# Performance work log

Hardware: AMD Instinct MI355X
Metric: run time of the kernel (lower is better)

## Reference

```python
import jax, jax.numpy as jnp
import numpy as np

# ---- static config (from MACEConfig / MACELayerConfig) ----
N_NODES = 128
F_S = 128          # n_invariant_feat_hidden (0e channels)
F_V = 64           # n_vectors_hidden (1e channels)
N_BESSEL = 8       # bessel_number
R_MAX = 5.0        # r_max
N_LAYERS = 2       # n_interactions
HID_RAD = 64       # radial MLP hidden width
F_S_OUT = 128      # n_invariant_feat_readout
F_V_OUT = 64       # n_vectors_readout
AVG_NEIGH = float(N_NODES)  # avg_num_neighbors default = n_nodes
RAD_OUT = F_S + 3 * F_V     # per-edge radial channel weights for the 4 TP paths


def _senders_receivers(n):
    # fully connected graph, matching get_senders_and_receivers
    s = np.repeat(np.arange(n), n - 1)
    j = np.tile(np.arange(1, n), n)
    r = (s + j) % n
    return jnp.asarray(s, dtype=jnp.int32), jnp.asarray(r, dtype=jnp.int32)


def _bessel(r):
    # e3nn bessel basis: sqrt(2/c) sin(n pi r / c) / r, n = 1..N_BESSEL
    n = jnp.arange(1, N_BESSEL + 1, dtype=r.dtype)
    return jnp.sqrt(2.0 / R_MAX) * jnp.sin(n * jnp.pi * r[:, None] / R_MAX) / r[:, None]


def _envelope(r):
    # smooth radial cutoff (polynomial p=6), stand-in for e3nn soft_envelope
    u = r / R_MAX
    p = 6.0
    env = 1.0 - (p + 1) * (p + 2) / 2 * u ** p + p * (p + 2) * u ** (p + 1) - p * (p + 1) / 2 * u ** (p + 2)
    return jnp.where(u < 1.0, env, 0.0)


def _forward(x, species_embed, Wr1, Wr2, W_sv, W_mix_s, W_mix_v, W_out_s, W_out_v):
    senders, receivers = _senders_receivers(N_NODES)

    def single(pos):  # pos: (N, 3)
        com = pos.mean(axis=0)                       # centre of mass (3,)
        v = pos[receivers] - pos[senders]            # edge relative vectors (E, 3)
        r = jnp.linalg.norm(v, axis=-1) + 1e-8       # (E,)
        vhat = v / r[:, None]
        rb = _bessel(r) * _envelope(r)[:, None]      # (E, N_BESSEL)

        s = jnp.broadcast_to(species_embed[0], (N_NODES, F_S))       # 0e node feats
        V = jnp.zeros((N_NODES, F_V, 3), dtype=pos.dtype)            # 1e node feats

        for l in range(N_LAYERS):
            # learned per-edge radial weights for each tensor-product path
            h = jax.nn.silu(rb @ Wr1[l]) @ Wr2[l]    # (E, RAD_OUT)
            R0 = h[:, :F_S]
            R1 = h[:, F_S:F_S + F_V]
            R2 = h[:, F_S + F_V:F_S + 2 * F_V]
            R3 = h[:, F_S + 2 * F_V:]

            s_src = s[senders]                       # gather (E, F_S)
            V_src = V[senders]                       # gather (E, F_V, 3)

            # CG tensor-product paths (only 0e and 1e irreps present):
            m0a = R0 * s_src                                         # 0e x 0e -> 0e
            m0b = R1 * jnp.einsum('efk,ek->ef', V_src, vhat)         # 1e x 1e -> 0e
            m1a = (R2 * (s_src @ W_sv[l]))[..., None] * vhat[:, None, :]  # 0e x 1e -> 1e
            m1b = R3[..., None] * V_src                              # 1e x 0e -> 1e

            # scatter-sum message passing over receivers
            agg0 = jax.ops.segment_sum(jnp.concatenate([m0a, m0b], -1), receivers,
                                       num_segments=N_NODES) / AVG_NEIGH   # (N, F_S+F_V)
            agg1 = jax.ops.segment_sum(jnp.concatenate([m1a, m1b], 1), receivers,
                                       num_segments=N_NODES) / AVG_NEIGH   # (N, 2F_V, 3)

            s = s + jax.nn.silu(agg0 @ W_mix_s[l])
            V = V + jnp.einsum('nfk,fg->ngk', agg1, W_mix_v[l])

        out_s = s @ W_out_s                                          # (N, F_S_OUT)
        out_v = jnp.einsum('nfk,fg->ngk', V, W_out_v) + com          # (N, F_V_OUT, 3) + CoM
        return out_v, out_s

    return jax.vmap(single)(x)


def setup_inputs() -> dict:
    key = jax.random.key(0)
    ks = jax.random.split(key, 10)
    sc = lambda fan: 1.0 / np.sqrt(fan)
    inp = {
        'x': jax.random.normal(ks[0], (8, N_NODES, 3), dtype=jnp.float32),
        'species_embed': jax.random.normal(ks[1], (1, F_S), dtype=jnp.float32),
        'Wr1': jax.random.normal(ks[2], (N_LAYERS, N_BESSEL, HID_RAD), dtype=jnp.float32) * sc(N_BESSEL),
        'Wr2': jax.random.normal(ks[3], (N_LAYERS, HID_RAD, RAD_OUT), dtype=jnp.float32) * sc(HID_RAD),
        'W_sv': jax.random.normal(ks[4], (N_LAYERS, F_S, F_V), dtype=jnp.float32) * sc(F_S),
        'W_mix_s': jax.random.normal(ks[5], (N_LAYERS, F_S + F_V, F_S), dtype=jnp.float32) * sc(F_S + F_V),
        'W_mix_v': jax.random.normal(ks[6], (N_LAYERS, 2 * F_V, F_V), dtype=jnp.float32) * sc(2 * F_V),
        'W_out_s': jax.random.normal(ks[7], (F_S, F_S_OUT), dtype=jnp.float32) * sc(F_S),
        'W_out_v': jax.random.normal(ks[8], (F_V, F_V_OUT), dtype=jnp.float32) * sc(F_V),
    }
    return inp


def reference(x, species_embed, Wr1, Wr2, W_sv, W_mix_s, W_mix_v, W_out_s, W_out_v):
    return _forward(x, species_embed, Wr1, Wr2, W_sv, W_mix_s, W_mix_v, W_out_s, W_out_v)
```

## Files before the change

kernel.cpp:

```cpp
#include <hip/hip_runtime.h>
#include <math.h>

typedef unsigned short u16;
typedef __attribute__((ext_vector_type(8))) short frag_ab;
typedef __attribute__((ext_vector_type(4))) float frag_cd;

#define BATCH 8
#define NN 128
#define FS 128
#define FV 64
#define NB 8
#define HID 64
#define ROUT 320
#define HSTRB 72

#define SZ_S (BATCH*FS*NN)
#define SZ_V (BATCH*FV*3*NN)
#define SZ_T (BATCH*FV*NN)
#define N_W2B (ROUT*HID)
#define OFF_SB 0
#define OFF_VB (OFF_SB+SZ_S)
#define OFF_T1 (OFF_VB+SZ_V)
#define OFF_W2B (OFF_T1+SZ_T)

// ... 154 lines not shown
    const int g = tid - 320;
    float a0=0.f, a1=0.f;
    #pragma unroll 8
    for (int c=0; c<FS; c+=2){
      a0 = fmaf(species[c],   Wsv[c*FV+g],     a0);
      a1 = fmaf(species[c+1], Wsv[(c+1)*FV+g], a1);
    }
    t0L[g] = a0+a1;
  } else if (tid < 424){
    const int t = blockIdx.x*40 + (tid-384);
    const int j = t & 63, c = t >> 6;
    w2b[t] = f2bf(Wr2[HID*ROUT + j*ROUT + c]);
  }
  __syncthreads();

  if (tid < FS){
    float a0=0.f, a1=0.f;
    #pragma unroll 2
    for (int c0=0; c0<128; c0+=4){
      float4 g0 = *(const float4*)&aggS[0][c0];
      float4 g1 = *(const float4*)&aggS[1][c0];
      float w0 = WmixSl[c0*FS+tid];
      float w1 = WmixSl[(c0+1)*FS+tid];
      float w2 = WmixSl[(c0+2)*FS+tid];
      float w3 = WmixSl[(c0+3)*FS+tid];
      a0 = fmaf(g0.x,w0,a0); a0 = fmaf(g0.y,w1,a0); a0 = fmaf(g0.z,w2,a0); a0 = fmaf(g0.w,w3,a0);
      a1 = fmaf(g1.x,w0,a1); a1 = fmaf(g1.y,w1,a1); a1 = fmaf(g1.z,w2,a1); a1 = fmaf(g1.w,w3,a1);
    }
    float sn0 = species[tid] + silu_f(a0);
    float sn1 = species[tid] + silu_f(a1);
    sNew[0][tid] = sn0;
    sNew[1][tid] = sn1;
    sOut[(b*FS+tid)*NN + k0]     = sn0;
    sOut[(b*FS+tid)*NN + k0 + 1] = sn1;
  } else if (tid < 320){
    const int o = tid - 128;
    const int g = o/3, c3 = o - g*3;
    float a0=0.f, a1=0.f;
    #pragma unroll 2
    for (int f0=0; f0<FV; f0+=4){
      float4 dv0 = *(const float4*)&dV[0][c3*68+f0];
      float4 dv1 = *(const float4*)&dV[1][c3*68+f0];
      float4 t4  = *(const float4*)&t0L[f0];
      float w0 = WmixVl[f0*FV+g];
      float w1 = WmixVl[(f0+1)*FV+g];
      float w2 = WmixVl[(f0+2)*FV+g];
      float w3 = WmixVl[(f0+3)*FV+g];
      a0 = fmaf(t4.x*dv0.x, w0, a0); a0 = fmaf(t4.y*dv0.y, w1, a0);
      a0 = fmaf(t4.z*dv0.z, w2, a0); a0 = fmaf(t4.w*dv0.w, w3, a0);
      a1 = fmaf(t4.x*dv1.x, w0, a1); a1 = fmaf(t4.y*dv1.y, w1, a1);
      a1 = fmaf(t4.z*dv1.z, w2, a1); a1 = fmaf(t4.w*dv1.w, w3, a1);
    }
    vOut[(b*FV*3 + o)*NN + k0]     = a0;
    vOut[(b*FV*3 + o)*NN + k0 + 1] = a1;
  }
  __syncthreads();

  if (tid < 256){
    const int g = tid & 63, p = tid >> 6;
    const float* Wsv1 = Wsv + FS*FV;
    const int f0 = p*32;
    float a0=0.f, a1=0.f;
    #pragma unroll 2
    for (int f=f0; f<f0+32; f+=4){
      float4 s0 = *(const float4*)&sNew[0][f];
      float4 s1 = *(const float4*)&sNew[1][f];
      float w0 = Wsv1[f*FV+g];
      float w1 = Wsv1[(f+1)*FV+g];
      float w2 = Wsv1[(f+2)*FV+g];
      float w3 = Wsv1[(f+3)*FV+g];
      a0 = fmaf(s0.x,w0,a0); a0 = fmaf(s0.y,w1,a0); a0 = fmaf(s0.z,w2,a0); a0 = fmaf(s0.w,w3,a0);
      a1 = fmaf(s1.x,w0,a1); a1 = fmaf(s1.y,w1,a1); a1 = fmaf(s1.z,w2,a1); a1 = fmaf(s1.w,w3,a1);
    }
    tPart[p][0][g] = a0; tPart[p][1][g] = a1;
  }
  __syncthreads();
  if (tid < 128){
    const int g = tid & 63, kk = tid >> 6;
    tOut[(b*FV+g)*NN + k0 + kk] =
        tPart[0][kk][g] + tPart[1][kk][g] + tPart[2][kk][g] + tPart[3][kk][g];
  }
}

__global__ __launch_bounds__(1024, 4) void layer_kernel(
    const float* __restrict__ pos,
    const float* __restrict__ sIn,
    const float* __restrict__ vIn,
    const float* __restrict__ tIn,
    const float* __restrict__ Wr1l,
    const u16*   __restrict__ w2bl,
    const float* __restrict__ WmixSl,
    const float* __restrict__ WmixVl,
    const float* __restrict__ WoutS,
    const float* __restrict__ WoutV,
    float* __restrict__ outp)
{
  const int tid  = threadIdx.x;
  const int b    = blockIdx.x >> 5;
  const int k0   = (blockIdx.x & 31) * 4;
  const int w    = tid >> 6;
  const int lane = tid & 63;
  const int col  = lane & 15;
  const int quad = lane >> 4;
  const int gh   = w & 1;
  const int wq   = (w >> 1) & 3;
  const int sh   = w >> 3;

  __shared__ u16   hidB[4][128*HSTRB];
  __shared__ float vhx[4][128], vhy[4][128], vhz[4][128];
  __shared__ float aggP[4][2][600];
  __shared__ float sPart[4][4][FS];
  __shared__ float sNew[4][FS];
  __shared__ float vNewL[4][204];
  __shared__ float comL[3];

  const float* pb = pos + b*NN*3;

  {
    const int jh = tid >> 9;
    const int kk = (tid >> 7) & 3;
    const int i  = tid & 127;
    const int k  = k0 + kk;
    float vx = pb[k*3+0]-pb[i*3+0];
    float vy = pb[k*3+1]-pb[i*3+1];
    float vz = pb[k*3+2]-pb[i*3+2];
    float r = sqrtf(vx*vx+vy*vy+vz*vz) + 1e-8f;
    float inv = 1.0f/r;
    if (jh == 0){ vhx[kk][i]=vx*inv; vhy[kk][i]=vy*inv; vhz[kk][i]=vz*inv; }
    float u = r*0.2f;
    float env = 0.0f;
    if (u < 1.0f && i != k){
      float u2=u*u, u6=u2*u2*u2;
      env = 1.0f - 28.0f*u6 + 48.0f*u6*u - 21.0f*u6*u2;
    }
    float coef = 0.6324555320336759f * inv * env;
    float th   = r * 0.6283185307179586f;
    float s1 = __sinf(th), c1 = __cosf(th);
    float rb[NB];
    rb[0] = coef*s1;
    float twoc = 2.f*c1, sp = s1, spp = 0.f;
    #pragma unroll
    for(int n=1;n<NB;n++){ float s = twoc*sp - spp; spp = sp; sp = s; rb[n] = coef*s; }
    u16* hrow = hidB[kk] + i*HSTRB;
    #pragma unroll
    for(int jg0=0;jg0<8;jg0++){
      const int jg = jh*8 + jg0;
      float h0=0.f,h1=0.f,h2=0.f,h3=0.f;
      #pragma unroll
      for(int n=0;n<NB;n++){
        const float* wr = Wr1l + n*HID + jg*4;
        float rn = rb[n];
        h0 = fmaf(rn, wr[0], h0);
        h1 = fmaf(rn, wr[1], h1);
        h2 = fmaf(rn, wr[2], h2);
        h3 = fmaf(rn, wr[3], h3);
      }
      ushort4 uu = make_ushort4(f2bf(silu_f(h0)), f2bf(silu_f(h1)),
                                f2bf(silu_f(h2)), f2bf(silu_f(h3)));
      *(ushort4*)(hrow + jg*4) = uu;
    }
    if (tid < 3){
      float a0=0.f, a1=0.f;
      for (int n=0;n<NN;n+=2){ a0 += pb[n*3+tid]; a1 += pb[(n+1)*3+tid]; }
      comL[tid] = (a0+a1) * (1.0f/128.0f);
    }
  }
  __syncthreads();

  const float* sIb = sIn + b*FS*NN;
  const float* vIb = vIn + b*FV*3*NN;
  const float* tIb = tIn + b*FV*NN;
  const int i00 = sh*64 + quad*4;

  if (gh == 0){
    const int c_s0 = wq*16 + col;
    const int c_s1 = 64 + c_s0;

    const u16* wp0 = w2bl + c_s0*HID + quad*8;
    const u16* wp1 = w2bl + c_s1*HID + quad*8;
    const u16* wp2 = w2bl + (128 + c_s0)*HID + quad*8;
    const frag_ab b00 = *(const frag_ab*)(wp0), b01 = *(const frag_ab*)(wp0+32);
    const frag_ab b10 = *(const frag_ab*)(wp1), b11 = *(const frag_ab*)(wp1+32);
    const frag_ab b20 = *(const frag_ab*)(wp2), b21 = *(const frag_ab*)(wp2+32);

    const float* fs0 = sIb + c_s0*NN + i00;
    const float* fs1 = sIb + c_s1*NN + i00;
    const float* fv  = vIb + c_s0*3*NN + i00;

    float sA0[4]={0.f,0.f,0.f,0.f}, sA1[4]={0.f,0.f,0.f,0.f}, sA2[4]={0.f,0.f,0.f,0.f};

    #pragma unroll 1
    for (int mt=0; mt<4; mt++){
      float4 s4a = *(const float4*)&fs0[mt*16];
      float4 s4b = *(const float4*)&fs1[mt*16];
      float4 vx4 = *(const float4*)&fv[mt*16];
      float4 vy4 = *(const float4*)&fv[NN + mt*16];
      float4 vz4 = *(const float4*)&fv[2*NN + mt*16];
      const int hbase = (sh*64 + mt*16 + col)*HSTRB + quad*8;
      const int vbase = i00 + mt*16;
      #pragma unroll
      for (int kk=0; kk<4; kk++){
        frag_ab a0 = *(const frag_ab*)&hidB[kk][hbase];
        frag_ab a1 = *(const frag_ab*)&hidB[kk][hbase + 32];
        float4 hx4 = *(const float4*)&vhx[kk][vbase];
        float4 hy4 = *(const float4*)&vhy[kk][vbase];
        float4 hz4 = *(const float4*)&vhz[kk][vbase];
        frag_cd ac0 = {0.f,0.f,0.f,0.f};
        frag_cd ac1 = {0.f,0.f,0.f,0.f};
        frag_cd ac2 = {0.f,0.f,0.f,0.f};
        ac0 = __builtin_amdgcn_mfma_f32_16x16x32_bf16(a0, b00, ac0, 0,0,0);
        ac1 = __builtin_amdgcn_mfma_f32_16x16x32_bf16(a0, b10, ac1, 0,0,0);
        ac2 = __builtin_amdgcn_mfma_f32_16x16x32_bf16(a0, b20, ac2, 0,0,0);
        ac0 = __builtin_amdgcn_mfma_f32_16x16x32_bf16(a1, b01, ac0, 0,0,0);
        ac1 = __builtin_amdgcn_mfma_f32_16x16x32_bf16(a1, b11, ac1, 0,0,0);
        ac2 = __builtin_amdgcn_mfma_f32_16x16x32_bf16(a1, b21, ac2, 0,0,0);

        sA0[kk] += ac0[0]*s4a.x + ac0[1]*s4a.y + ac0[2]*s4a.z + ac0[3]*s4a.w;
        sA1[kk] += ac1[0]*s4b.x + ac1[1]*s4b.y + ac1[2]*s4b.z + ac1[3]*s4b.w;
        sA2[kk] += ac2[0]*(vx4.x*hx4.x + vy4.x*hy4.x + vz4.x*hz4.x)
                 + ac2[1]*(vx4.y*hx4.y + vy4.y*hy4.y + vz4.y*hz4.y)
                 + ac2[2]*(vx4.z*hx4.z + vy4.z*hy4.z + vz4.z*hz4.z)
                 + ac2[3]*(vx4.w*hx4.w + vy4.w*hy4.w + vz4.w*hz4.w);
      }
    }
    #pragma unroll
    for (int kk=0; kk<4; kk++){
      float v0 = sA0[kk]; v0 += __shfl_xor(v0,16,64); v0 += __shfl_xor(v0,32,64);
      float v1 = sA1[kk]; v1 += __shfl_xor(v1,16,64); v1 += __shfl_xor(v1,32,64);
      float v2 = sA2[kk]; v2 += __shfl_xor(v2,16,64); v2 += __shfl_xor(v2,32,64);
      if (lane < 16){
        aggP[kk][sh][wq*16 + lane]       = v0;
        aggP[kk][sh][64 + wq*16 + lane]  = v1;
        aggP[kk][sh][128 + wq*16 + lane] = v2;
      }
    }
  } else {
    const int f_vc = wq*16 + col;

    const u16* wp3 = w2bl + (192 + f_vc)*HID + quad*8;
    const u16* wp4 = w2bl + (256 + f_vc)*HID + quad*8;
    const frag_ab b30 = *(const frag_ab*)(wp3), b31 = *(const frag_ab*)(wp3+32);
    const frag_ab b40 = *(const frag_ab*)(wp4), b41 = *(const frag_ab*)(wp4+32);

    const float* fv = vIb + f_vc*3*NN + i00;
    const float* ft = tIb + f_vc*NN + i00;

    float sX3[4]={0.f,0.f,0.f,0.f}, sY3[4]={0.f,0.f,0.f,0.f}, sZ3[4]={0.f,0.f,0.f,0.f};
    float sX4[4]={0.f,0.f,0.f,0.f}, sY4[4]={0.f,0.f,0.f,0.f}, sZ4[4]={0.f,0.f,0.f,0.f};

    #pragma unroll 1
    for (int mt=0; mt<4; mt++){
      float4 vx4 = *(const float4*)&fv[mt*16];
      float4 vy4 = *(const float4*)&fv[NN + mt*16];
      float4 vz4 = *(const float4*)&fv[2*NN + mt*16];
      float4 t4  = *(const float4*)&ft[mt*16];
      const int hbase = (sh*64 + mt*16 + col)*HSTRB + quad*8;
      const int vbase = i00 + mt*16;
      #pragma unroll
      for (int kk=0; kk<4; kk++){
        frag_ab a0 = *(const frag_ab*)&hidB[kk][hbase];
        frag_ab a1 = *(const frag_ab*)&hidB[kk][hbase + 32];
        float4 hx4 = *(const float4*)&vhx[kk][vbase];
        float4 hy4 = *(const float4*)&vhy[kk][vbase];
        float4 hz4 = *(const float4*)&vhz[kk][vbase];
        frag_cd ac3 = {0.f,0.f,0.f,0.f};
        frag_cd ac4 = {0.f,0.f,0.f,0.f};
        ac3 = __builtin_amdgcn_mfma_f32_16x16x32_bf16(a0, b30, ac3, 0,0,0);
        ac4 = __builtin_amdgcn_mfma_f32_16x16x32_bf16(a0, b40, ac4, 0,0,0);
        ac3 = __builtin_amdgcn_mfma_f32_16x16x32_bf16(a1, b31, ac3, 0,0,0);
        ac4 = __builtin_amdgcn_mfma_f32_16x16x32_bf16(a1, b41, ac4, 0,0,0);

        float t0_ = ac3[0]*t4.x, t1_ = ac3[1]*t4.y, t2_ = ac3[2]*t4.z, t3_ = ac3[3]*t4.w;
        sX3[kk] += t0_*hx4.x + t1_*hx4.y + t2_*hx4.z + t3_*hx4.w;
        sY3[kk] += t0_*hy4.x + t1_*hy4.y + t2_*hy4.z + t3_*hy4.w;
        sZ3[kk] += t0_*hz4.x + t1_*hz4.y + t2_*hz4.z + t3_*hz4.w;
        sX4[kk] += ac4[0]*vx4.x + ac4[1]*vx4.y + ac4[2]*vx4.z + ac4[3]*vx4.w;
        sY4[kk] += ac4[0]*vy4.x + ac4[1]*vy4.y + ac4[2]*vy4.z + ac4[3]*vy4.w;
        sZ4[kk] += ac4[0]*vz4.x + ac4[1]*vz4.y + ac4[2]*vz4.z + ac4[3]*vz4.w;
      }
    }
    #pragma unroll
    for (int kk=0; kk<4; kk++){
      float x3 = sX3[kk]; x3 += __shfl_xor(x3,16,64); x3 += __shfl_xor(x3,32,64);
      float y3 = sY3[kk]; y3 += __shfl_xor(y3,16,64); y3 += __shfl_xor(y3,32,64);
      float z3 = sZ3[kk]; z3 += __shfl_xor(z3,16,64); z3 += __shfl_xor(z3,32,64);
      float x4 = sX4[kk]; x4 += __shfl_xor(x4,16,64); x4 += __shfl_xor(x4,32,64);
      float y4 = sY4[kk]; y4 += __shfl_xor(y4,16,64); y4 += __shfl_xor(y4,32,64);
      float z4 = sZ4[kk]; z4 += __shfl_xor(z4,16,64); z4 += __shfl_xor(z4,32,64);
      if (lane < 16){
        const int f2 = wq*16 + lane;
        aggP[kk][sh][192       + f2] = x3;
        aggP[kk][sh][192 +  68 + f2] = y3;
        aggP[kk][sh][192 + 136 + f2] = z3;
        aggP[kk][sh][396       + f2] = x4;
        aggP[kk][sh][396 +  68 + f2] = y4;
        aggP[kk][sh][396 + 136 + f2] = z4;
      }
    }
  }

  __syncthreads();
  for (int t2=tid; t2<2400; t2+=1024){
    const int kk = t2 / 600;
    const int t  = t2 - kk*600;
    aggP[kk][0][t] = (aggP[kk][0][t] + aggP[kk][1][t]) * (1.0f/128.0f);
  }
  __syncthreads();

  if (tid < 512){
    const int o = tid & 127, p = tid >> 7;
    const int c0 = p*48;
    float a0=0.f,a1=0.f,a2=0.f,a3=0.f;
    #pragma unroll 2
    for (int cc=c0; cc<c0+48; cc+=4){
      float4 g0 = *(const float4*)&aggP[0][0][cc];
      float4 g1 = *(const float4*)&aggP[1][0][cc];
      float4 g2 = *(const float4*)&aggP[2][0][cc];
      float4 g3 = *(const float4*)&aggP[3][0][cc];
      float w0 = WmixSl[cc*FS+o];
      float w1 = WmixSl[(cc+1)*FS+o];
      float w2 = WmixSl[(cc+2)*FS+o];
      float w3 = WmixSl[(cc+3)*FS+o];
      a0 = fmaf(g0.x,w0,a0); a0 = fmaf(g0.y,w1,a0); a0 = fmaf(g0.z,w2,a0); a0 = fmaf(g0.w,w3,a0);
      a1 = fmaf(g1.x,w0,a1); a1 = fmaf(g1.y,w1,a1); a1 = fmaf(g1.z,w2,a1); a1 = fmaf(g1.w,w3,a1);
      a2 = fmaf(g2.x,w0,a2); a2 = fmaf(g2.y,w1,a2); a2 = fmaf(g2.z,w2,a2); a2 = fmaf(g2.w,w3,a2);
      a3 = fmaf(g3.x,w0,a3); a3 = fmaf(g3.y,w1,a3); a3 = fmaf(g3.z,w2,a3); a3 = fmaf(g3.w,w3,a3);
    }
    sPart[0][p][o] = a0; sPart[1][p][o] = a1;
    sPart[2][p][o] = a2; sPart[3][p][o] = a3;
  } else if (tid < 704){
    const int o = tid - 512;
    const int c3 = o >> 6, g = o & 63;
    float a0=0.f,a1=0.f,a2=0.f,a3=0.f;
    #pragma unroll 1
    for (int f0=0; f0<FV; f0+=4){
      float4 p0 = *(const float4*)&aggP[0][0][192+c3*68+f0];
      float4 q0 = *(const float4*)&aggP[0][0][396+c3*68+f0];
      float4 p1 = *(const float4*)&aggP[1][0][192+c3*68+f0];
      float4 q1 = *(const float4*)&aggP[1][0][396+c3*68+f0];
      float4 p2 = *(const float4*)&aggP[2][0][192+c3*68+f0];
      float4 q2 = *(const float4*)&aggP[2][0][396+c3*68+f0];
      float4 p3 = *(const float4*)&aggP[3][0][192+c3*68+f0];
      float4 q3 = *(const float4*)&aggP[3][0][396+c3*68+f0];
      float w00 = WmixVl[f0*FV+g];
      float w01 = WmixVl[(f0+1)*FV+g];
      float w02 = WmixVl[(f0+2)*FV+g];
      float w03 = WmixVl[(f0+3)*FV+g];
      float w10 = WmixVl[(f0+FV)*FV+g];
      float w11 = WmixVl[(f0+FV+1)*FV+g];
      float w12 = WmixVl[(f0+FV+2)*FV+g];
      float w13 = WmixVl[(f0+FV+3)*FV+g];
      a0 = fmaf(p0.x,w00,a0); a0 = fmaf(p0.y,w01,a0); a0 = fmaf(p0.z,w02,a0); a0 = fmaf(p0.w,w03,a0);
      a0 = fmaf(q0.x,w10,a0); a0 = fmaf(q0.y,w11,a0); a0 = fmaf(q0.z,w12,a0); a0 = fmaf(q0.w,w13,a0);
      a1 = fmaf(p1.x,w00,a1); a1 = fmaf(p1.y,w01,a1); a1 = fmaf(p1.z,w02,a1); a1 = fmaf(p1.w,w03,a1);
      a1 = fmaf(q1.x,w10,a1); a1 = fmaf(q1.y,w11,a1); a1 = fmaf(q1.z,w12,a1); a1 = fmaf(q1.w,w13,a1);
      a2 = fmaf(p2.x,w00,a2); a2 = fmaf(p2.y,w01,a2); a2 = fmaf(p2.z,w02,a2); a2 = fmaf(p2.w,w03,a2);
      a2 = fmaf(q2.x,w10,a2); a2 = fmaf(q2.y,w11,a2); a2 = fmaf(q2.z,w12,a2); a2 = fmaf(q2.w,w13,a2);
      a3 = fmaf(p3.x,w00,a3); a3 = fmaf(p3.y,w01,a3); a3 = fmaf(p3.z,w02,a3); a3 = fmaf(p3.w,w03,a3);
      a3 = fmaf(q3.x,w10,a3); a3 = fmaf(q3.y,w11,a3); a3 = fmaf(q3.z,w12,a3); a3 = fmaf(q3.w,w13,a3);
    }
    const int oo = g*3 + c3;
    vNewL[0][c3*68+g] = vIb[oo*NN + k0]     + a0;
    vNewL[1][c3*68+g] = vIb[oo*NN + k0 + 1] + a1;
    vNewL[2][c3*68+g] = vIb[oo*NN + k0 + 2] + a2;
    vNewL[3][c3*68+g] = vIb[oo*NN + k0 + 3] + a3;
  }
  __syncthreads();

  if (tid < FS){
    #pragma unroll
    for (int kk=0; kk<4; kk++)
      sNew[kk][tid] = sIb[tid*NN + k0 + kk]
                    + silu_f(sPart[kk][0][tid] + sPart[kk][1][tid]
                           + sPart[kk][2][tid] + sPart[kk][3][tid]);
  } else if (tid < 320){
    const int o = tid - 128;
    const int g = o/3, c3 = o - g*3;
    float a0 = comL[c3], a1 = comL[c3], a2 = comL[c3], a3 = comL[c3];
    #pragma unroll 2
    for (int f0=0; f0<FV; f0+=4){
      float4 v0 = *(const float4*)&vNewL[0][c3*68+f0];
      float4 v1 = *(const float4*)&vNewL[1][c3*68+f0];
      float4 v2 = *(const float4*)&vNewL[2][c3*68+f0];
      float4 v3 = *(const float4*)&vNewL[3][c3*68+f0];
      float w0 = WoutV[f0*FV+g];
      float w1 = WoutV[(f0+1)*FV+g];
      float w2 = WoutV[(f0+2)*FV+g];
      float w3 = WoutV[(f0+3)*FV+g];
      a0 = fmaf(v0.x,w0,a0); a0 = fmaf(v0.y,w1,a0); a0 = fmaf(v0.z,w2,a0); a0 = fmaf(v0.w,w3,a0);
      a1 = fmaf(v1.x,w0,a1); a1 = fmaf(v1.y,w1,a1); a1 = fmaf(v1.z,w2,a1); a1 = fmaf(v1.w,w3,a1);
      a2 = fmaf(v2.x,w0,a2); a2 = fmaf(v2.y,w1,a2); a2 = fmaf(v2.z,w2,a2); a2 = fmaf(v2.w,w3,a2);
      a3 = fmaf(v3.x,w0,a3); a3 = fmaf(v3.y,w1,a3); a3 = fmaf(v3.z,w2,a3); a3 = fmaf(v3.w,w3,a3);
    }
    outp[(b*NN+k0)*FV*3 + o]   = a0;
    outp[(b*NN+k0+1)*FV*3 + o] = a1;
    outp[(b*NN+k0+2)*FV*3 + o] = a2;
    outp[(b*NN+k0+3)*FV*3 + o] = a3;
  }
  __syncthreads();

  float* e3s = &aggP[0][0][0];
  if (tid < 512){
    const int o = tid & 127, p = tid >> 7;
    const int f0 = p*32;
    float a0=0.f,a1=0.f,a2=0.f,a3=0.f;
    #pragma unroll 2
    for (int f=f0; f<f0+32; f+=4){
      float4 s0 = *(const float4*)&sNew[0][f];
      float4 s1 = *(const float4*)&sNew[1][f];
      float4 s2 = *(const float4*)&sNew[2][f];
      float4 s3 = *(const float4*)&sNew[3][f];
      float w0 = WoutS[f*FS+o];
      float w1 = WoutS[(f+1)*FS+o];
      float w2 = WoutS[(f+2)*FS+o];
      float w3 = WoutS[(f+3)*FS+o];
      a0 = fmaf(s0.x,w0,a0); a0 = fmaf(s0.y,w1,a0); a0 = fmaf(s0.z,w2,a0); a0 = fmaf(s0.w,w3,a0);
      a1 = fmaf(s1.x,w0,a1); a1 = fmaf(s1.y,w1,a1); a1 = fmaf(s1.z,w2,a1); a1 = fmaf(s1.w,w3,a1);
      a2 = fmaf(s2.x,w0,a2); a2 = fmaf(s2.y,w1,a2); a2 = fmaf(s2.z,w2,a2); a2 = fmaf(s2.w,w3,a2);
      a3 = fmaf(s3.x,w0,a3); a3 = fmaf(s3.y,w1,a3); a3 = fmaf(s3.z,w2,a3); a3 = fmaf(s3.w,w3,a3);
    }
    e3s[(p*4+0)*128 + o] = a0;
    e3s[(p*4+1)*128 + o] = a1;
    e3s[(p*4+2)*128 + o] = a2;
    e3s[(p*4+3)*128 + o] = a3;
  }
  __syncthreads();

  if (tid < 512){
    const int o = tid & 127, kk = tid >> 7;
    float a = e3s[(0*4+kk)*128 + o] + e3s[(1*4+kk)*128 + o]
            + e3s[(2*4+kk)*128 + o] + e3s[(3*4+kk)*128 + o];
    outp[BATCH*NN*FV*3 + (b*NN+k0+kk)*FS + o] = a;
  }
}

extern "C" void kernel_launch(void* const* d_in, const int* in_sizes, int n_in,
                              void* d_out, int out_size, void* d_ws, size_t ws_size,
                              hipStream_t stream)
{
  const float* x       = (const float*)d_in[0];
  const float* species = (const float*)d_in[1];
  const float* Wr1     = (const float*)d_in[2];
  const float* Wr2     = (const float*)d_in[3];
  const float* Wsv     = (const float*)d_in[4];
  const float* WmixS   = (const float*)d_in[5];
  const float* WmixV   = (const float*)d_in[6];
  const float* WoutS   = (const float*)d_in[7];
  const float* WoutV   = (const float*)d_in[8];
  float* ws  = (float*)d_ws;
  float* out = (float*)d_out;

  float* sB  = ws + OFF_SB;
  float* vB  = ws + OFF_VB;
  float* t1  = ws + OFF_T1;
  u16*   w2b = (u16*)(ws + OFF_W2B);

  layer0_kernel<<<BATCH*NN/2, 512, 0, stream>>>(x, species, Wr1, Wr2, Wsv,
      WmixS, WmixV, sB, vB, t1, w2b);

  layer_kernel<<<BATCH*NN/4, 1024, 0, stream>>>(x, sB, vB, t1,
      Wr1 + NB*HID, w2b, WmixS + 192*FS, WmixV + 128*FV,
      WoutS, WoutV, out);
}
```

Before: 127.9 us.

## Split layer kernel into 512-thread blocks handling two receivers each

The second-layer kernel now gives each block 2 receiver nodes instead of 4, using 512 threads and twice as many blocks. Each wave walks all 128 senders itself, so the split over sender halves and the shared-memory reduction pass with its extra barrier are removed. Shared memory per block drops, which may let more blocks fit per CU and spread work across more CUs. In exchange, each W2 bf16 fragment and the node features are loaded by twice as many blocks, and each wave runs a longer serial loop.

```diff
diff --git a/kernel.cpp b/kernel.cpp
--- a/kernel.cpp
+++ b/kernel.cpp
@@ -260,7 +260,7 @@
   }
 }
 
-__global__ __launch_bounds__(1024, 4) void layer_kernel(
+__global__ __launch_bounds__(512, 4) void layer_kernel(
     const float* __restrict__ pos,
     const float* __restrict__ sIn,
     const float* __restrict__ vIn,
@@ -274,37 +274,37 @@
     float* __restrict__ outp)
 {
   const int tid  = threadIdx.x;
-  const int b    = blockIdx.x >> 5;
-  const int k0   = (blockIdx.x & 31) * 4;
+  const int b    = blockIdx.x >> 6;
+  const int k0   = (blockIdx.x & 63) * 2;
   const int w    = tid >> 6;
   const int lane = tid & 63;
   const int col  = lane & 15;
   const int quad = lane >> 4;
   const int gh   = w & 1;
-  const int wq   = (w >> 1) & 3;
-  const int sh   = w >> 3;
-
-  __shared__ u16   hidB[4][128*HSTRB];
-  __shared__ float vhx[4][128], vhy[4][128], vhz[4][128];
-  __shared__ float aggP[4][2][600];
-  __shared__ float sPart[4][4][FS];
-  __shared__ float sNew[4][FS];
-  __shared__ float vNewL[4][204];
+  const int wq   = w >> 1;
+
+  __shared__ u16   hidB[2][128*HSTRB];
+  __shared__ float vhx[2][128], vhy[2][128], vhz[2][128];
+  __shared__ float aggP[2][600];
+  __shared__ float sPart[2][2][FS];
+  __shared__ float sNew[2][FS];
+  __shared__ float vNewL[2][204];
   __shared__ float comL[3];
 
   const float* pb = pos + b*NN*3;
 
   {
-    const int jh = tid >> 9;
-    const int kk = (tid >> 7) & 3;
-    const int i  = tid & 127;
-    const int k  = k0 + kk;
+    const int kk   = tid >> 8;
+    const int r2   = tid & 255;
+    const int i    = r2 & 127;
+    const int half = r2 >> 7;
+    const int k    = k0 + kk;
     float vx = pb[k*3+0]-pb[i*3+0];
     float vy = pb[k*3+1]-pb[i*3+1];
     float vz = pb[k*3+2]-pb[i*3+2];
     float r = sqrtf(vx*vx+vy*vy+vz*vz) + 1e-8f;
     float inv = 1.0f/r;
-    if (jh == 0){ vhx[kk][i]=vx*inv; vhy[kk][i]=vy*inv; vhz[kk][i]=vz*inv; }
+    if (half==0){ vhx[kk][i]=vx*inv; vhy[kk][i]=vy*inv; vhz[kk][i]=vz*inv; }
     float u = r*0.2f;
     float env = 0.0f;
     if (u < 1.0f && i != k){
@@ -322,7 +322,7 @@
     u16* hrow = hidB[kk] + i*HSTRB;
     #pragma unroll
     for(int jg0=0;jg0<8;jg0++){
-      const int jg = jh*8 + jg0;
+      const int jg = half*8 + jg0;
       float h0=0.f,h1=0.f,h2=0.f,h3=0.f;
       #pragma unroll
       for(int n=0;n<NB;n++){
@@ -348,7 +348,7 @@
   const float* sIb = sIn + b*FS*NN;
   const float* vIb = vIn + b*FV*3*NN;
   const float* tIb = tIn + b*FV*NN;
-  const int i00 = sh*64 + quad*4;
+  const int i00 = quad*4;
 
   if (gh == 0){
     const int c_s0 = wq*16 + col;
@@ -365,19 +365,19 @@
     const float* fs1 = sIb + c_s1*NN + i00;
     const float* fv  = vIb + c_s0*3*NN + i00;
 
-    float sA0[4]={0.f,0.f,0.f,0.f}, sA1[4]={0.f,0.f,0.f,0.f}, sA2[4]={0.f,0.f,0.f,0.f};
+    float sA0[2]={0.f,0.f}, sA1[2]={0.f,0.f}, sA2[2]={0.f,0.f};
 
     #pragma unroll 1
-    for (int mt=0; mt<4; mt++){
+    for (int mt=0; mt<8; mt++){
       float4 s4a = *(const float4*)&fs0[mt*16];
       float4 s4b = *(const float4*)&fs1[mt*16];
       float4 vx4 = *(const float4*)&fv[mt*16];
       float4 vy4 = *(const float4*)&fv[NN + mt*16];
       float4 vz4 = *(const float4*)&fv[2*NN + mt*16];
-      const int hbase = (sh*64 + mt*16 + col)*HSTRB + quad*8;
+      const int hbase = (mt*16 + col)*HSTRB + quad*8;
       const int vbase = i00 + mt*16;
       #pragma unroll
-      for (int kk=0; kk<4; kk++){
+      for (int kk=0; kk<2; kk++){
         frag_ab a0 = *(const frag_ab*)&hidB[kk][hbase];
         frag_ab a1 = *(const frag_ab*)&hidB[kk][hbase + 32];
         float4 hx4 = *(const float4*)&vhx[kk][vbase];
@@ -402,14 +402,14 @@
       }
     }
     #pragma unroll
-    for (int kk=0; kk<4; kk++){
+    for (int kk=0; kk<2; kk++){
       float v0 = sA0[kk]; v0 += __shfl_xor(v0,16,64); v0 += __shfl_xor(v0,32,64);
       float v1 = sA1[kk]; v1 += __shfl_xor(v1,16,64); v1 += __shfl_xor(v1,32,64);
       float v2 = sA2[kk]; v2 += __shfl_xor(v2,16,64); v2 += __shfl_xor(v2,32,64);
       if (lane < 16){
-        aggP[kk][sh][wq*16 + lane]       = v0;
-        aggP[kk][sh][64 + wq*16 + lane]  = v1;
-        aggP[kk][sh][128 + wq*16 + lane] = v2;
+        aggP[kk][wq*16 + lane]       = v0 * (1.0f/128.0f);
+        aggP[kk][64 + wq*16 + lane]  = v1 * (1.0f/128.0f);
+        aggP[kk][128 + wq*16 + lane] = v2 * (1.0f/128.0f);
       }
     }
   } else {
@@ -423,19 +423,19 @@
     const float* fv = vIb + f_vc*3*NN + i00;
     const float* ft = tIb + f_vc*NN + i00;
 
-    float sX3[4]={0.f,0.f,0.f,0.f}, sY3[4]={0.f,0.f,0.f,0.f}, sZ3[4]={0.f,0.f,0.f,0.f};
-    float sX4[4]={0.f,0.f,0.f,0.f}, sY4[4]={0.f,0.f,0.f,0.f}, sZ4[4]={0.f,0.f,0.f,0.f};
+    float sX3[2]={0.f,0.f}, sY3[2]={0.f,0.f}, sZ3[2]={0.f,0.f};
+    float sX4[2]={0.f,0.f}, sY4[2]={0.f,0.f}, sZ4[2]={0.f,0.f};
 
     #pragma unroll 1
-    for (int mt=0; mt<4; mt++){
+    for (int mt=0; mt<8; mt++){
       float4 vx4 = *(const float4*)&fv[mt*16];
       float4 vy4 = *(const float4*)&fv[NN + mt*16];
       float4 vz4 = *(const float4*)&fv[2*NN + mt*16];
       float4 t4  = *(const float4*)&ft[mt*16];
-      const int hbase = (sh*64 + mt*16 + col)*HSTRB + quad*8;
+      const int hbase = (mt*16 + col)*HSTRB + quad*8;
       const int vbase = i00 + mt*16;
       #pragma unroll
-      for (int kk=0; kk<4; kk++){
+      for (int kk=0; kk<2; kk++){
         frag_ab a0 = *(const frag_ab*)&hidB[kk][hbase];
         frag_ab a1 = *(const frag_ab*)&hidB[kk][hbase + 32];
         float4 hx4 = *(const float4*)&vhx[kk][vbase];
@@ -458,7 +458,7 @@
       }
     }
     #pragma unroll
-    for (int kk=0; kk<4; kk++){
+    for (int kk=0; kk<2; kk++){
       float x3 = sX3[kk]; x3 += __shfl_xor(x3,16,64); x3 += __shfl_xor(x3,32,64);
       float y3 = sY3[kk]; y3 += __shfl_xor(y3,16,64); y3 += __shfl_xor(y3,32,64);
       float z3 = sZ3[kk]; z3 += __shfl_xor(z3,16,64); z3 += __shfl_xor(z3,32,64);
@@ -467,59 +467,43 @@
       float z4 = sZ4[kk]; z4 += __shfl_xor(z4,16,64); z4 += __shfl_xor(z4,32,64);
       if (lane < 16){
         const int f2 = wq*16 + lane;
-        aggP[kk][sh][192       + f2] = x3;
-        aggP[kk][sh][192 +  68 + f2] = y3;
-        aggP[kk][sh][192 + 136 + f2] = z3;
-        aggP[kk][sh][396       + f2] = x4;
-        aggP[kk][sh][396 +  68 + f2] = y4;
-        aggP[kk][sh][396 + 136 + f2] = z4;
-      }
-    }
-  }
-
-  __syncthreads();
-  for (int t2=tid; t2<2400; t2+=1024){
-    const int kk = t2 / 600;
-    const int t  = t2 - kk*600;
-    aggP[kk][0][t] = (aggP[kk][0][t] + aggP[kk][1][t]) * (1.0f/128.0f);
-  }
-  __syncthreads();
-
-  if (tid < 512){
+        aggP[kk][192       + f2] = x3 * (1.0f/128.0f);
+        aggP[kk][192 +  68 + f2] = y3 * (1.0f/128.0f);
+        aggP[kk][192 + 136 + f2] = z3 * (1.0f/128.0f);
+        aggP[kk][396       + f2] = x4 * (1.0f/128.0f);
+        aggP[kk][396 +  68 + f2] = y4 * (1.0f/128.0f);
+        aggP[kk][396 + 136 + f2] = z4 * (1.0f/128.0f);
+      }
+    }
+  }
+  __syncthreads();
+
+  if (tid < 256){
     const int o = tid & 127, p = tid >> 7;
-    const int c0 = p*48;
-    float a0=0.f,a1=0.f,a2=0.f,a3=0.f;
-    #pragma unroll 2
-    for (int cc=c0; cc<c0+48; cc+=4){
-      float4 g0 = *(const float4*)&aggP[0][0][cc];
-      float4 g1 = *(const float4*)&aggP[1][0][cc];
-      float4 g2 = *(const float4*)&aggP[2][0][cc];
-      float4 g3 = *(const float4*)&aggP[3][0][cc];
+    const int c0 = p*96;
+    float a0=0.f,a1=0.f;
+    #pragma unroll 2
+    for (int cc=c0; cc<c0+96; cc+=4){
+      float4 g0 = *(const float4*)&aggP[0][cc];
+      float4 g1 = *(const float4*)&aggP[1][cc];
       float w0 = WmixSl[cc*FS+o];
       float w1 = WmixSl[(cc+1)*FS+o];
       float w2 = WmixSl[(cc+2)*FS+o];
       float w3 = WmixSl[(cc+3)*FS+o];
       a0 = fmaf(g0.x,w0,a0); a0 = fmaf(g0.y,w1,a0); a0 = fmaf(g0.z,w2,a0); a0 = fmaf(g0.w,w3,a0);
       a1 = fmaf(g1.x,w0,a1); a1 = fmaf(g1.y,w1,a1); a1 = fmaf(g1.z,w2,a1); a1 = fmaf(g1.w,w3,a1);
-      a2 = fmaf(g2.x,w0,a2); a2 = fmaf(g2.y,w1,a2); a2 = fmaf(g2.z,w2,a2); a2 = fmaf(g2.w,w3,a2);
-      a3 = fmaf(g3.x,w0,a3); a3 = fmaf(g3.y,w1,a3); a3 = fmaf(g3.z,w2,a3); a3 = fmaf(g3.w,w3,a3);
     }
     sPart[0][p][o] = a0; sPart[1][p][o] = a1;
-    sPart[2][p][o] = a2; sPart[3][p][o] = a3;
-  } else if (tid < 704){
-    const int o = tid - 512;
+  } else if (tid < 448){
+    const int o = tid - 256;
     const int c3 = o >> 6, g = o & 63;
-    float a0=0.f,a1=0.f,a2=0.f,a3=0.f;
+    float a0=0.f,a1=0.f;
     #pragma unroll 1
     for (int f0=0; f0<FV; f0+=4){
-      float4 p0 = *(const float4*)&aggP[0][0][192+c3*68+f0];
-      float4 q0 = *(const float4*)&aggP[0][0][396+c3*68+f0];
-      float4 p1 = *(const float4*)&aggP[1][0][192+c3*68+f0];
-      float4 q1 = *(const float4*)&aggP[1][0][396+c3*68+f0];
-      float4 p2 = *(const float4*)&aggP[2][0][192+c3*68+f0];
-      float4 q2 = *(const float4*)&aggP[2][0][396+c3*68+f0];
-      float4 p3 = *(const float4*)&aggP[3][0][192+c3*68+f0];
-      float4 q3 = *(const float4*)&aggP[3][0][396+c3*68+f0];
+      float4 p0 = *(const float4*)&aggP[0][192+c3*68+f0];
+      float4 q0 = *(const float4*)&aggP[0][396+c3*68+f0];
+      float4 p1 = *(const float4*)&aggP[1][192+c3*68+f0];
+      float4 q1 = *(const float4*)&aggP[1][396+c3*68+f0];
       float w00 = WmixVl[f0*FV+g];
       float w01 = WmixVl[(f0+1)*FV+g];
       float w02 = WmixVl[(f0+2)*FV+g];
@@ -532,82 +516,62 @@
       a0 = fmaf(q0.x,w10,a0); a0 = fmaf(q0.y,w11,a0); a0 = fmaf(q0.z,w12,a0); a0 = fmaf(q0.w,w13,a0);
       a1 = fmaf(p1.x,w00,a1); a1 = fmaf(p1.y,w01,a1); a1 = fmaf(p1.z,w02,a1); a1 = fmaf(p1.w,w03,a1);
       a1 = fmaf(q1.x,w10,a1); a1 = fmaf(q1.y,w11,a1); a1 = fmaf(q1.z,w12,a1); a1 = fmaf(q1.w,w13,a1);
-      a2 = fmaf(p2.x,w00,a2); a2 = fmaf(p2.y,w01,a2); a2 = fmaf(p2.z,w02,a2); a2 = fmaf(p2.w,w03,a2);
-      a2 = fmaf(q2.x,w10,a2); a2 = fmaf(q2.y,w11,a2); a2 = fmaf(q2.z,w12,a2); a2 = fmaf(q2.w,w13,a2);
-      a3 = fmaf(p3.x,w00,a3); a3 = fmaf(p3.y,w01,a3); a3 = fmaf(p3.z,w02,a3); a3 = fmaf(p3.w,w03,a3);
-      a3 = fmaf(q3.x,w10,a3); a3 = fmaf(q3.y,w11,a3); a3 = fmaf(q3.z,w12,a3); a3 = fmaf(q3.w,w13,a3);
     }
     const int oo = g*3 + c3;
     vNewL[0][c3*68+g] = vIb[oo*NN + k0]     + a0;
     vNewL[1][c3*68+g] = vIb[oo*NN + k0 + 1] + a1;
-    vNewL[2][c3*68+g] = vIb[oo*NN + k0 + 2] + a2;
-    vNewL[3][c3*68+g] = vIb[oo*NN + k0 + 3] + a3;
   }
   __syncthreads();
 
   if (tid < FS){
     #pragma unroll
-    for (int kk=0; kk<4; kk++)
+    for (int kk=0; kk<2; kk++)
       sNew[kk][tid] = sIb[tid*NN + k0 + kk]
-                    + silu_f(sPart[kk][0][tid] + sPart[kk][1][tid]
-                           + sPart[kk][2][tid] + sPart[kk][3][tid]);
+                    + silu_f(sPart[kk][0][tid] + sPart[kk][1][tid]);
   } else if (tid < 320){
     const int o = tid - 128;
     const int g = o/3, c3 = o - g*3;
-    float a0 = comL[c3], a1 = comL[c3], a2 = comL[c3], a3 = comL[c3];
+    float a0 = comL[c3], a1 = comL[c3];
     #pragma unroll 2
     for (int f0=0; f0<FV; f0+=4){
       float4 v0 = *(const float4*)&vNewL[0][c3*68+f0];
       float4 v1 = *(const float4*)&vNewL[1][c3*68+f0];
-      float4 v2 = *(const float4*)&vNewL[2][c3*68+f0];
-      float4 v3 = *(const float4*)&vNewL[3][c3*68+f0];
       float w0 = WoutV[f0*FV+g];
       float w1 = WoutV[(f0+1)*FV+g];
       float w2 = WoutV[(f0+2)*FV+g];
       float w3 = WoutV[(f0+3)*FV+g];
       a0 = fmaf(v0.x,w0,a0); a0 = fmaf(v0.y,w1,a0); a0 = fmaf(v0.z,w2,a0); a0 = fmaf(v0.w,w3,a0);
       a1 = fmaf(v1.x,w0,a1); a1 = fmaf(v1.y,w1,a1); a1 = fmaf(v1.z,w2,a1); a1 = fmaf(v1.w,w3,a1);
-      a2 = fmaf(v2.x,w0,a2); a2 = fmaf(v2.y,w1,a2); a2 = fmaf(v2.z,w2,a2); a2 = fmaf(v2.w,w3,a2);
-      a3 = fmaf(v3.x,w0,a3); a3 = fmaf(v3.y,w1,a3); a3 = fmaf(v3.z,w2,a3); a3 = fmaf(v3.w,w3,a3);
     }
     outp[(b*NN+k0)*FV*3 + o]   = a0;
     outp[(b*NN+k0+1)*FV*3 + o] = a1;
-    outp[(b*NN+k0+2)*FV*3 + o] = a2;
-    outp[(b*NN+k0+3)*FV*3 + o] = a3;
-  }
-  __syncthreads();
-
-  float* e3s = &aggP[0][0][0];
-  if (tid < 512){
+  }
+  __syncthreads();
+
+  float* e3s = &aggP[0][0];
+  if (tid < 256){
     const int o = tid & 127, p = tid >> 7;
-    const int f0 = p*32;
-    float a0=0.f,a1=0.f,a2=0.f,a3=0.f;
-    #pragma unroll 2
-    for (int f=f0; f<f0+32; f+=4){
+    const int f0 = p*64;
+    float a0=0.f,a1=0.f;
+    #pragma unroll 2
+    for (int f=f0; f<f0+64; f+=4){
       float4 s0 = *(const float4*)&sNew[0][f];
       float4 s1 = *(const float4*)&sNew[1][f];
-      float4 s2 = *(const float4*)&sNew[2][f];
-      float4 s3 = *(const float4*)&sNew[3][f];
       float w0 = WoutS[f*FS+o];
       float w1 = WoutS[(f+1)*FS+o];
       float w2 = WoutS[(f+2)*FS+o];
       float w3 = WoutS[(f+3)*FS+o];
       a0 = fmaf(s0.x,w0,a0); a0 = fmaf(s0.y,w1,a0); a0 = fmaf(s0.z,w2,a0); a0 = fmaf(s0.w,w3,a0);
       a1 = fmaf(s1.x,w0,a1); a1 = fmaf(s1.y,w1,a1); a1 = fmaf(s1.z,w2,a1); a1 = fmaf(s1.w,w3,a1);
-      a2 = fmaf(s2.x,w0,a2); a2 = fmaf(s2.y,w1,a2); a2 = fmaf(s2.z,w2,a2); a2 = fmaf(s2.w,w3,a2);
-      a3 = fmaf(s3.x,w0,a3); a3 = fmaf(s3.y,w1,a3); a3 = fmaf(s3.z,w2,a3); a3 = fmaf(s3.w,w3,a3);
-    }
-    e3s[(p*4+0)*128 + o] = a0;
-    e3s[(p*4+1)*128 + o] = a1;
-    e3s[(p*4+2)*128 + o] = a2;
-    e3s[(p*4+3)*128 + o] = a3;
-  }
-  __syncthreads();
-
-  if (tid < 512){
+    }
+    e3s[(p*2+0)*128 + o] = a0;
+    e3s[(p*2+1)*128 + o] = a1;
+  }
+  __syncthreads();
+
+  if (tid < 256){
     const int o = tid & 127, kk = tid >> 7;
-    float a = e3s[(0*4+kk)*128 + o] + e3s[(1*4+kk)*128 + o]
-            + e3s[(2*4+kk)*128 + o] + e3s[(3*4+kk)*128 + o];
+    float a = e3s[(0*2+kk)*128 + o] + e3s[(1*2+kk)*128 + o];
     outp[BATCH*NN*FV*3 + (b*NN+k0+kk)*FS + o] = a;
   }
 }
@@ -636,7 +600,7 @@
   layer0_kernel<<<BATCH*NN/2, 512, 0, stream>>>(x, species, Wr1, Wr2, Wsv,
       WmixS, WmixV, sB, vB, t1, w2b);
 
-  layer_kernel<<<BATCH*NN/4, 1024, 0, stream>>>(x, sB, vB, t1,
+  layer_kernel<<<BATCH*NN/2, 512, 0, stream>>>(x, sB, vB, t1,
       Wr1 + NB*HID, w2b, WmixS + 192*FS, WmixV + 128*FV,
       WoutS, WoutV, out);
 }
```

Result: no change. 130.0 us (+1.6%).

## Halve layer_kernel block size by merging scalar and vector TP paths per wave

Applied to the files above, without the earlier changes.

Shrinks layer_kernel from 1024 to 512 threads per block. Each wave now computes all five tensor-product paths (scalar, vector and both 1e outputs) instead of splitting them across two wave groups, and each thread now computes all 64 hidden radial features. The reduction stages are re-split to fit 512 threads. The aim is less per-block thread overhead and shared B-fragment and activation reuse within a wave. The cost is higher register pressure and more serial work per wave, with fewer waves available to hide latency.

```diff
diff --git a/kernel.cpp b/kernel.cpp
--- a/kernel.cpp
+++ b/kernel.cpp
@@ -260,7 +260,7 @@
   }
 }
 
-__global__ __launch_bounds__(1024, 4) void layer_kernel(
+__global__ __launch_bounds__(512, 2) void layer_kernel(
     const float* __restrict__ pos,
     const float* __restrict__ sIn,
     const float* __restrict__ vIn,
@@ -280,14 +280,13 @@
   const int lane = tid & 63;
   const int col  = lane & 15;
   const int quad = lane >> 4;
-  const int gh   = w & 1;
-  const int wq   = (w >> 1) & 3;
-  const int sh   = w >> 3;
+  const int wq   = w & 3;
+  const int sh   = w >> 2;
 
   __shared__ u16   hidB[4][128*HSTRB];
   __shared__ float vhx[4][128], vhy[4][128], vhz[4][128];
   __shared__ float aggP[4][2][600];
-  __shared__ float sPart[4][4][FS];
+  __shared__ float sPart[4][2][FS];
   __shared__ float sNew[4][FS];
   __shared__ float vNewL[4][204];
   __shared__ float comL[3];
@@ -295,8 +294,7 @@
   const float* pb = pos + b*NN*3;
 
   {
-    const int jh = tid >> 9;
-    const int kk = (tid >> 7) & 3;
+    const int kk = tid >> 7;
     const int i  = tid & 127;
     const int k  = k0 + kk;
     float vx = pb[k*3+0]-pb[i*3+0];
@@ -304,7 +302,7 @@
     float vz = pb[k*3+2]-pb[i*3+2];
     float r = sqrtf(vx*vx+vy*vy+vz*vz) + 1e-8f;
     float inv = 1.0f/r;
-    if (jh == 0){ vhx[kk][i]=vx*inv; vhy[kk][i]=vy*inv; vhz[kk][i]=vz*inv; }
+    vhx[kk][i]=vx*inv; vhy[kk][i]=vy*inv; vhz[kk][i]=vz*inv;
     float u = r*0.2f;
     float env = 0.0f;
     if (u < 1.0f && i != k){
@@ -321,8 +319,7 @@
     for(int n=1;n<NB;n++){ float s = twoc*sp - spp; spp = sp; sp = s; rb[n] = coef*s; }
     u16* hrow = hidB[kk] + i*HSTRB;
     #pragma unroll
-    for(int jg0=0;jg0<8;jg0++){
-      const int jg = jh*8 + jg0;
+    for(int jg=0;jg<16;jg++){
       float h0=0.f,h1=0.f,h2=0.f,h3=0.f;
       #pragma unroll
       for(int n=0;n<NB;n++){
@@ -350,84 +347,35 @@
   const float* tIb = tIn + b*FV*NN;
   const int i00 = sh*64 + quad*4;
 
-  if (gh == 0){
+  {
     const int c_s0 = wq*16 + col;
     const int c_s1 = 64 + c_s0;
+    const int f_vc = c_s0;
 
     const u16* wp0 = w2bl + c_s0*HID + quad*8;
     const u16* wp1 = w2bl + c_s1*HID + quad*8;
-    const u16* wp2 = w2bl + (128 + c_s0)*HID + quad*8;
+    const u16* wp2 = w2bl + (128 + f_vc)*HID + quad*8;
+    const u16* wp3 = w2bl + (192 + f_vc)*HID + quad*8;
+    const u16* wp4 = w2bl + (256 + f_vc)*HID + quad*8;
     const frag_ab b00 = *(const frag_ab*)(wp0), b01 = *(const frag_ab*)(wp0+32);
     const frag_ab b10 = *(const frag_ab*)(wp1), b11 = *(const frag_ab*)(wp1+32);
     const frag_ab b20 = *(const frag_ab*)(wp2), b21 = *(const frag_ab*)(wp2+32);
+    const frag_ab b30 = *(const frag_ab*)(wp3), b31 = *(const frag_ab*)(wp3+32);
+    const frag_ab b40 = *(const frag_ab*)(wp4), b41 = *(const frag_ab*)(wp4+32);
 
     const float* fs0 = sIb + c_s0*NN + i00;
     const float* fs1 = sIb + c_s1*NN + i00;
-    const float* fv  = vIb + c_s0*3*NN + i00;
+    const float* fv  = vIb + f_vc*3*NN + i00;
+    const float* ft  = tIb + f_vc*NN + i00;
 
     float sA0[4]={0.f,0.f,0.f,0.f}, sA1[4]={0.f,0.f,0.f,0.f}, sA2[4]={0.f,0.f,0.f,0.f};
+    float sX3[4]={0.f,0.f,0.f,0.f}, sY3[4]={0.f,0.f,0.f,0.f}, sZ3[4]={0.f,0.f,0.f,0.f};
+    float sX4[4]={0.f,0.f,0.f,0.f}, sY4[4]={0.f,0.f,0.f,0.f}, sZ4[4]={0.f,0.f,0.f,0.f};
 
     #pragma unroll 1
     for (int mt=0; mt<4; mt++){
       float4 s4a = *(const float4*)&fs0[mt*16];
       float4 s4b = *(const float4*)&fs1[mt*16];
-      float4 vx4 = *(const float4*)&fv[mt*16];
-      float4 vy4 = *(const float4*)&fv[NN + mt*16];
-      float4 vz4 = *(const float4*)&fv[2*NN + mt*16];
-      const int hbase = (sh*64 + mt*16 + col)*HSTRB + quad*8;
-      const int vbase = i00 + mt*16;
-      #pragma unroll
-      for (int kk=0; kk<4; kk++){
-        frag_ab a0 = *(const frag_ab*)&hidB[kk][hbase];
-        frag_ab a1 = *(const frag_ab*)&hidB[kk][hbase + 32];
-        float4 hx4 = *(const float4*)&vhx[kk][vbase];
-        float4 hy4 = *(const float4*)&vhy[kk][vbase];
-        float4 hz4 = *(const float4*)&vhz[kk][vbase];
-        frag_cd ac0 = {0.f,0.f,0.f,0.f};
-        frag_cd ac1 = {0.f,0.f,0.f,0.f};
-        frag_cd ac2 = {0.f,0.f,0.f,0.f};
-        ac0 = __builtin_amdgcn_mfma_f32_16x16x32_bf16(a0, b00, ac0, 0,0,0);
-        ac1 = __builtin_amdgcn_mfma_f32_16x16x32_bf16(a0, b10, ac1, 0,0,0);
-        ac2 = __builtin_amdgcn_mfma_f32_16x16x32_bf16(a0, b20, ac2, 0,0,0);
-        ac0 = __builtin_amdgcn_mfma_f32_16x16x32_bf16(a1, b01, ac0, 0,0,0);
-        ac1 = __builtin_amdgcn_mfma_f32_16x16x32_bf16(a1, b11, ac1, 0,0,0);
-        ac2 = __builtin_amdgcn_mfma_f32_16x16x32_bf16(a1, b21, ac2, 0,0,0);
-
-        sA0[kk] += ac0[0]*s4a.x + ac0[1]*s4a.y + ac0[2]*s4a.z + ac0[3]*s4a.w;
-        sA1[kk] += ac1[0]*s4b.x + ac1[1]*s4b.y + ac1[2]*s4b.z + ac1[3]*s4b.w;
-        sA2[kk] += ac2[0]*(vx4.x*hx4.x + vy4.x*hy4.x + vz4.x*hz4.x)
-                 + ac2[1]*(vx4.y*hx4.y + vy4.y*hy4.y + vz4.y*hz4.y)
-                 + ac2[2]*(vx4.z*hx4.z + vy4.z*hy4.z + vz4.z*hz4.z)
-                 + ac2[3]*(vx4.w*hx4.w + vy4.w*hy4.w + vz4.w*hz4.w);
-      }
-    }
-    #pragma unroll
-    for (int kk=0; kk<4; kk++){
-      float v0 = sA0[kk]; v0 += __shfl_xor(v0,16,64); v0 += __shfl_xor(v0,32,64);
-      float v1 = sA1[kk]; v1 += __shfl_xor(v1,16,64); v1 += __shfl_xor(v1,32,64);
-      float v2 = sA2[kk]; v2 += __shfl_xor(v2,16,64); v2 += __shfl_xor(v2,32,64);
-      if (lane < 16){
-        aggP[kk][sh][wq*16 + lane]       = v0;
-        aggP[kk][sh][64 + wq*16 + lane]  = v1;
-        aggP[kk][sh][128 + wq*16 + lane] = v2;
-      }
-    }
-  } else {
-    const int f_vc = wq*16 + col;
-
-    const u16* wp3 = w2bl + (192 + f_vc)*HID + quad*8;
-    const u16* wp4 = w2bl + (256 + f_vc)*HID + quad*8;
-    const frag_ab b30 = *(const frag_ab*)(wp3), b31 = *(const frag_ab*)(wp3+32);
-    const frag_ab b40 = *(const frag_ab*)(wp4), b41 = *(const frag_ab*)(wp4+32);
-
-    const float* fv = vIb + f_vc*3*NN + i00;
-    const float* ft = tIb + f_vc*NN + i00;
-
-    float sX3[4]={0.f,0.f,0.f,0.f}, sY3[4]={0.f,0.f,0.f,0.f}, sZ3[4]={0.f,0.f,0.f,0.f};
-    float sX4[4]={0.f,0.f,0.f,0.f}, sY4[4]={0.f,0.f,0.f,0.f}, sZ4[4]={0.f,0.f,0.f,0.f};
-
-    #pragma unroll 1
-    for (int mt=0; mt<4; mt++){
       float4 vx4 = *(const float4*)&fv[mt*16];
       float4 vy4 = *(const float4*)&fv[NN + mt*16];
       float4 vz4 = *(const float4*)&fv[2*NN + mt*16];
@@ -441,13 +389,28 @@
         float4 hx4 = *(const float4*)&vhx[kk][vbase];
         float4 hy4 = *(const float4*)&vhy[kk][vbase];
         float4 hz4 = *(const float4*)&vhz[kk][vbase];
+        frag_cd ac0 = {0.f,0.f,0.f,0.f};
+        frag_cd ac1 = {0.f,0.f,0.f,0.f};
+        frag_cd ac2 = {0.f,0.f,0.f,0.f};
         frag_cd ac3 = {0.f,0.f,0.f,0.f};
         frag_cd ac4 = {0.f,0.f,0.f,0.f};
+        ac0 = __builtin_amdgcn_mfma_f32_16x16x32_bf16(a0, b00, ac0, 0,0,0);
+        ac1 = __builtin_amdgcn_mfma_f32_16x16x32_bf16(a0, b10, ac1, 0,0,0);
+        ac2 = __builtin_amdgcn_mfma_f32_16x16x32_bf16(a0, b20, ac2, 0,0,0);
         ac3 = __builtin_amdgcn_mfma_f32_16x16x32_bf16(a0, b30, ac3, 0,0,0);
         ac4 = __builtin_amdgcn_mfma_f32_16x16x32_bf16(a0, b40, ac4, 0,0,0);
+        ac0 = __builtin_amdgcn_mfma_f32_16x16x32_bf16(a1, b01, ac0, 0,0,0);
+        ac1 = __builtin_amdgcn_mfma_f32_16x16x32_bf16(a1, b11, ac1, 0,0,0);
+        ac2 = __builtin_amdgcn_mfma_f32_16x16x32_bf16(a1, b21, ac2, 0,0,0);
         ac3 = __builtin_amdgcn_mfma_f32_16x16x32_bf16(a1, b31, ac3, 0,0,0);
         ac4 = __builtin_amdgcn_mfma_f32_16x16x32_bf16(a1, b41, ac4, 0,0,0);
 
+        sA0[kk] += ac0[0]*s4a.x + ac0[1]*s4a.y + ac0[2]*s4a.z + ac0[3]*s4a.w;
+        sA1[kk] += ac1[0]*s4b.x + ac1[1]*s4b.y + ac1[2]*s4b.z + ac1[3]*s4b.w;
+        sA2[kk] += ac2[0]*(vx4.x*hx4.x + vy4.x*hy4.x + vz4.x*hz4.x)
+                 + ac2[1]*(vx4.y*hx4.y + vy4.y*hy4.y + vz4.y*hz4.y)
+                 + ac2[2]*(vx4.z*hx4.z + vy4.z*hy4.z + vz4.z*hz4.z)
+                 + ac2[3]*(vx4.w*hx4.w + vy4.w*hy4.w + vz4.w*hz4.w);
         float t0_ = ac3[0]*t4.x, t1_ = ac3[1]*t4.y, t2_ = ac3[2]*t4.z, t3_ = ac3[3]*t4.w;
         sX3[kk] += t0_*hx4.x + t1_*hx4.y + t2_*hx4.z + t3_*hx4.w;
         sY3[kk] += t0_*hy4.x + t1_*hy4.y + t2_*hy4.z + t3_*hy4.w;
@@ -457,8 +420,12 @@
         sZ4[kk] += ac4[0]*vz4.x + ac4[1]*vz4.y + ac4[2]*vz4.z + ac4[3]*vz4.w;
       }
     }
+
     #pragma unroll
     for (int kk=0; kk<4; kk++){
+      float v0 = sA0[kk]; v0 += __shfl_xor(v0,16,64); v0 += __shfl_xor(v0,32,64);
+      float v1 = sA1[kk]; v1 += __shfl_xor(v1,16,64); v1 += __shfl_xor(v1,32,64);
+      float v2 = sA2[kk]; v2 += __shfl_xor(v2,16,64); v2 += __shfl_xor(v2,32,64);
       float x3 = sX3[kk]; x3 += __shfl_xor(x3,16,64); x3 += __shfl_xor(x3,32,64);
       float y3 = sY3[kk]; y3 += __shfl_xor(y3,16,64); y3 += __shfl_xor(y3,32,64);
       float z3 = sZ3[kk]; z3 += __shfl_xor(z3,16,64); z3 += __shfl_xor(z3,32,64);
@@ -466,6 +433,9 @@
       float y4 = sY4[kk]; y4 += __shfl_xor(y4,16,64); y4 += __shfl_xor(y4,32,64);
       float z4 = sZ4[kk]; z4 += __shfl_xor(z4,16,64); z4 += __shfl_xor(z4,32,64);
       if (lane < 16){
+        aggP[kk][sh][wq*16 + lane]        = v0;
+        aggP[kk][sh][64 + wq*16 + lane]   = v1;
+        aggP[kk][sh][128 + wq*16 + lane]  = v2;
         const int f2 = wq*16 + lane;
         aggP[kk][sh][192       + f2] = x3;
         aggP[kk][sh][192 +  68 + f2] = y3;
@@ -478,19 +448,19 @@
   }
 
   __syncthreads();
-  for (int t2=tid; t2<2400; t2+=1024){
+  for (int t2=tid; t2<2400; t2+=512){
     const int kk = t2 / 600;
     const int t  = t2 - kk*600;
     aggP[kk][0][t] = (aggP[kk][0][t] + aggP[kk][1][t]) * (1.0f/128.0f);
   }
   __syncthreads();
 
-  if (tid < 512){
+  if (tid < 256){
     const int o = tid & 127, p = tid >> 7;
-    const int c0 = p*48;
+    const int c0 = p*96;
     float a0=0.f,a1=0.f,a2=0.f,a3=0.f;
     #pragma unroll 2
-    for (int cc=c0; cc<c0+48; cc+=4){
+    for (int cc=c0; cc<c0+96; cc+=4){
       float4 g0 = *(const float4*)&aggP[0][0][cc];
       float4 g1 = *(const float4*)&aggP[1][0][cc];
       float4 g2 = *(const float4*)&aggP[2][0][cc];
@@ -506,8 +476,8 @@
     }
     sPart[0][p][o] = a0; sPart[1][p][o] = a1;
     sPart[2][p][o] = a2; sPart[3][p][o] = a3;
-  } else if (tid < 704){
-    const int o = tid - 512;
+  } else if (tid < 448){
+    const int o = tid - 256;
     const int c3 = o >> 6, g = o & 63;
     float a0=0.f,a1=0.f,a2=0.f,a3=0.f;
     #pragma unroll 1
@@ -549,8 +519,7 @@
     #pragma unroll
     for (int kk=0; kk<4; kk++)
       sNew[kk][tid] = sIb[tid*NN + k0 + kk]
-                    + silu_f(sPart[kk][0][tid] + sPart[kk][1][tid]
-                           + sPart[kk][2][tid] + sPart[kk][3][tid]);
+                    + silu_f(sPart[kk][0][tid] + sPart[kk][1][tid]);
   } else if (tid < 320){
     const int o = tid - 128;
     const int g = o/3, c3 = o - g*3;
@@ -636,7 +605,7 @@
   layer0_kernel<<<BATCH*NN/2, 512, 0, stream>>>(x, species, Wr1, Wr2, Wsv,
       WmixS, WmixV, sB, vB, t1, w2b);
 
-  layer_kernel<<<BATCH*NN/4, 1024, 0, stream>>>(x, sB, vB, t1,
+  layer_kernel<<<BATCH*NN/4, 512, 0, stream>>>(x, sB, vB, t1,
       Wr1 + NB*HID, w2b, WmixS + 192*FS, WmixV + 128*FV,
       WoutS, WoutV, out);
 }
```

New measurement: 127.1 us (median of 2 runs). Within noise of the previous version (-0.6%).
